# Kernel optimization log

Measured on AMD Instinct MI355X. Metric: run time of the kernel, lower is better.

The kernel has to match this reference:

```python
import jax, jax.numpy as jnp
import numpy as np

B, S, D, H = 4, 2048, 1024, 16
DK = D // H


def setup_inputs() -> dict:
    key = jax.random.key(0)
    ks = jax.random.split(key, 12)
    s = 1.0 / np.sqrt(D)
    return {
        "query": jax.random.normal(ks[0], (B, S, D), jnp.float32),
        "key": jax.random.normal(ks[1], (B, S, D), jnp.float32),
        "value": jax.random.normal(ks[2], (B, S, D), jnp.float32),
        "mask": jnp.ones((1, 1, S, S), jnp.int32),
        "w_q": jax.random.normal(ks[3], (D, D), jnp.float32) * s,
        "b_q": jax.random.normal(ks[4], (D,), jnp.float32) * s,
        "w_k": jax.random.normal(ks[5], (D, D), jnp.float32) * s,
        "b_k": jax.random.normal(ks[6], (D,), jnp.float32) * s,
        "w_v": jax.random.normal(ks[7], (D, D), jnp.float32) * s,
        "b_v": jax.random.normal(ks[8], (D,), jnp.float32) * s,
        "w_o": jax.random.normal(ks[9], (D, D), jnp.float32) * s,
        "b_o": jax.random.normal(ks[10], (D,), jnp.float32) * s,
    }


def reference(query, key, value, mask, w_q, b_q, w_k, b_k, w_v, b_v, w_o, b_o):
    # linear projections (torch Linear: x @ W^T + b)
    q = query @ w_q.T + b_q
    k = key @ w_k.T + b_k
    v = value @ w_v.T + b_v
    # [B, S, D] -> [B, H, S, DK]
    q = q.reshape(B, S, H, DK).transpose(0, 2, 1, 3)
    k = k.reshape(B, S, H, DK).transpose(0, 2, 1, 3)
    v = v.reshape(B, S, H, DK).transpose(0, 2, 1, 3)
    scores = jnp.einsum("bhqd,bhkd->bhqk", q, k) / jnp.sqrt(jnp.float32(DK))
    scores = jnp.where(mask == 0, jnp.float32(-1e9), scores)
    attn = jax.nn.softmax(scores, axis=-1)  # dropout p=0.0 -> identity
    x = jnp.einsum("bhqk,bhkd->bhqd", attn, v)
    x = x.transpose(0, 2, 1, 3).reshape(B, S, D)
    return x @ w_o.T + b_o
```

## Files before the change

kernel.cpp:

```cpp
#include <hip/hip_runtime.h>
#include <stdint.h>

#define S_LEN 2048
#define NHEAD 16
#define DHEAD 64
#define DMODEL 1024
#define MROWS 8192

typedef unsigned short ushort_t;
typedef __attribute__((ext_vector_type(8))) __bf16 bf16x8;
typedef __attribute__((ext_vector_type(4))) float f32x4;

__device__ __forceinline__ float bf2f(ushort_t h) {
    union { unsigned int u; float f; } v; v.u = ((unsigned int)h) << 16; return v.f;
}
__device__ __forceinline__ ushort_t f2bf(float f) {
    union { float f; unsigned int u; } v; v.f = f;
    unsigned int u = v.u + 0x7fffu + ((v.u >> 16) & 1u);
    return (ushort_t)(u >> 16);
}

__device__ __forceinline__ void gload_lds16(const void* g, void* l)
{
    auto* g1 = reinterpret_cast<const __attribute__((address_space(1))) void*>(
        reinterpret_cast<uintptr_t>(g));
    auto* l3 = reinterpret_cast<__attribute__((address_space(3))) void*>(
        reinterpret_cast<uintptr_t>(l));
    __builtin_amdgcn_global_load_lds(g1, l3, 16, 0, 0);
}

__global__ void detect_dtype(const unsigned int* __restrict__ q, int* __restrict__ flag)
{
    __shared__ int cnt;
    if (threadIdx.x == 0) cnt = 0;
    __syncthreads();
    int c = 0;
    for (int i = 0; i < 8; ++i) {
        const unsigned int w = q[threadIdx.x * 8 + i];
        const unsigned int lo = w & 0xffffu;
        const unsigned int e = (lo >> 7) & 0xffu;
        if (lo == 0u || (e >= 96u && e <= 160u)) ++c;
    }
    atomicAdd(&cnt, c);
    __syncthreads();
    if (threadIdx.x == 0) flag[0] = (cnt < 400) ? 1 : 0;
}

__global__ void mask_flags(const int* __restrict__ mask, int* __restrict__ flags)
{
    __shared__ int ok_s;
    if (threadIdx.x == 0) ok_s = 1;
    __syncthreads();
    const int t = blockIdx.x;
    const int tq = t >> 4, tk = t & 15;
    int ok = 1;
    for (int i = 0; i < 64; ++i) {
        const int idx = i * 256 + threadIdx.x;
        const int r = idx >> 7, c = idx & 127;
        if (mask[(size_t)(tq * 128 + r) * S_LEN + tk * 128 + c] == 0) { ok = 0; break; }
    }
    if (!ok) atomicAnd(&ok_s, 0);
    __syncthreads();
    if (threadIdx.x == 0) flags[t] = ok_s;
}

__device__ __forceinline__ float loadscal(const void* b, int i, bool f32)
{
    return f32 ? ((const float*)b)[i] : bf2f(((const ushort_t*)b)[i]);
}

__global__ __launch_bounds__(256)
void conv_bf16(const void* __restrict__ src, ushort_t* __restrict__ dst,
               int n8, const int* __restrict__ dflag, int fidx)
{
    const bool f32 = dflag[fidx] != 0;
    const int stride = gridDim.x * 256;
    for (int i = blockIdx.x * 256 + threadIdx.x; i < n8; i += stride) {
        if (f32) {
            const float4 a = ((const float4*)src)[2 * (size_t)i];
            const float4 b = ((const float4*)src)[2 * (size_t)i + 1];
            union { ushort_t u[8]; uint4 v; } p;
            p.u[0] = f2bf(a.x); p.u[1] = f2bf(a.y); p.u[2] = f2bf(a.z); p.u[3] = f2bf(a.w);
            p.u[4] = f2bf(b.x); p.u[5] = f2bf(b.y); p.u[6] = f2bf(b.z); p.u[7] = f2bf(b.w);
            ((uint4*)dst)[i] = p.v;
        } else {
            ((uint4*)dst)[i] = ((const uint4*)src)[i];
        }
    }
}

__device__ __forceinline__ void gemm_core(
    const ushort_t* __restrict__ A, const ushort_t* __restrict__ W,
    const void* __restrict__ bias, void* __restrict__ out,
    bool bf32, bool outf,
    ushort_t (&As)[3][128 * 32], ushort_t (&Bs)[3][128 * 32])
{
    constexpr int K = DMODEL, N = DMODEL;
    const int tid = threadIdx.x;
    const int lane = tid & 63;
    const int wave = tid >> 6;
    const int lrow = lane & 15, lq = lane >> 4;
    const int m0 = blockIdx.x * 128;
    const int n0 = blockIdx.y * 128;
    const int wr = (wave >> 1) * 64;
    const int wc = (wave & 1) * 64;

    const f32x4 zero4 = {0.f, 0.f, 0.f, 0.f};
    f32x4 acc[4][4];
#pragma unroll
    for (int i = 0; i < 4; ++i)
#pragma unroll
        for (int j = 0; j < 4; ++j) acc[i][j] = zero4;

    const int r0  = tid >> 2;
    const int cc0 = (tid & 3) * 8;
    const int lb  = wave * 64 * 8;
    const int lb1 = (wave * 64 + 256) * 8;

    auto stage = [&](int buf, int k0) __attribute__((always_inline)) {
        gload_lds16(&A[(size_t)(m0 + r0) * K + k0 + cc0],      &As[buf][lb]);
        gload_lds16(&A[(size_t)(m0 + r0 + 64) * K + k0 + cc0], &As[buf][lb1]);
        gload_lds16(&W[(size_t)(n0 + r0) * K + k0 + cc0],      &Bs[buf][lb]);
        gload_lds16(&W[(size_t)(n0 + r0 + 64) * K + k0 + cc0], &Bs[buf][lb1]);
    };
    auto compute = [&](int buf) __attribute__((always_inline)) {
        bf16x8 af[4], bfr[4];
#pragma unroll
        for (int t = 0; t < 4; ++t) {
            af[t]  = *(const bf16x8*)(&As[buf][(wr + t * 16 + lrow) * 32 + lq * 8]);
            bfr[t] = *(const bf16x8*)(&Bs[buf][(wc + t * 16 + lrow) * 32 + lq * 8]);
        }
        __builtin_amdgcn_s_setprio(1);
#pragma unroll
        for (int mt = 0; mt < 4; ++mt)
#pragma unroll
            for (int nt = 0; nt < 4; ++nt)
                acc[mt][nt] = __builtin_amdgcn_mfma_f32_16x16x32_bf16(
                    af[mt], bfr[nt], acc[mt][nt], 0, 0, 0);
        __builtin_amdgcn_s_setprio(0);
    };

    stage(0, 0);
    stage(1, 32);
    asm volatile("s_waitcnt vmcnt(4)" ::: "memory");
    __builtin_amdgcn_s_barrier();

#pragma unroll 1
    for (int tt = 0; tt < 32; ++tt) {
        if (tt < 30) stage((tt + 2) % 3, (tt + 2) * 32);
        compute(tt % 3);
        if (tt < 31) {
            if (tt < 30) asm volatile("s_waitcnt vmcnt(4)" ::: "memory");
            else         asm volatile("s_waitcnt vmcnt(0)" ::: "memory");
            __builtin_amdgcn_s_barrier();
        }
    }

#pragma unroll
    for (int nt = 0; nt < 4; ++nt) {
        const int n = n0 + wc + nt * 16 + lrow;
        const float bv = loadscal(bias, n, bf32);
#pragma unroll
        for (int mt = 0; mt < 4; ++mt) {
            const int mbase = m0 + wr + mt * 16 + lq * 4;
#pragma unroll
            for (int r = 0; r < 4; ++r) {
                const float v = acc[mt][nt][r] + bv;
                const size_t o = (size_t)(mbase + r) * N + n;
                if (outf) ((float*)out)[o] = v;
                else      ((ushort_t*)out)[o] = f2bf(v);
            }
        }
    }
}

__global__ __launch_bounds__(256, 3)
void gemm_bf16(const ushort_t* __restrict__ A, const ushort_t* __restrict__ W,
               const void* __restrict__ bias, void* __restrict__ out,
               const int* __restrict__ dflag, int outf)
{
    __shared__ ushort_t As[3][128 * 32];
    __shared__ ushort_t Bs[3][128 * 32];
    gemm_core(A, W, bias, out, dflag[1] != 0, outf != 0, As, Bs);
}

__global__ __launch_bounds__(256, 3)
void gemm_qk(const ushort_t* __restrict__ A0, const ushort_t* __restrict__ W0,
             const void* __restrict__ b0, void* __restrict__ o0,
             const ushort_t* __restrict__ A1, const ushort_t* __restrict__ W1,
             const void* __restrict__ b1, void* __restrict__ o1,
             const int* __restrict__ dflag)
{
    __shared__ ushort_t As[3][128 * 32];
    __shared__ ushort_t Bs[3][128 * 32];
    const bool z = blockIdx.z != 0;
    gemm_core(z ? A1 : A0, z ? W1 : W0, z ? b1 : b0, z ? o1 : o0,
              dflag[1] != 0, false, As, Bs);
}

__global__ __launch_bounds__(256, 2)
void attn_mfma(const ushort_t* __restrict__ Q, const ushort_t* __restrict__ K,
               const ushort_t* __restrict__ V, const int* __restrict__ mask,
               const int* __restrict__ flags, ushort_t* __restrict__ X)
{
    constexpr int KP = 72;
    constexpr int VP = 130;
    constexpr int PP = 68;
    constexpr float CEXP = 0.18033688f;
    __shared__ ushort_t Ks[128 * KP];
    __shared__ ushort_t VTs[64 * VP];
    __shared__ ushort_t Ps[4][32 * PP];

    const int tid = threadIdx.x;
    const int lane = tid & 63;
    const int wave = tid >> 6;
    const int lrow = lane & 15, lq = lane >> 4;
    const int bh = blockIdx.y, b = bh >> 4, h = bh & 15;
    const int q0 = blockIdx.x * 128;
    const int qw = q0 + wave * 32;
    const int coff = h * 64;
    const size_t rowb = (size_t)b * S_LEN;

    bf16x8 qf[2][2];
#pragma unroll
    for (int mt = 0; mt < 2; ++mt)
#pragma unroll
        for (int ks = 0; ks < 2; ++ks)
            qf[mt][ks] = *(const bf16x8*)(
                &Q[(rowb + qw + mt * 16 + lrow) * DMODEL + coff + ks * 32 + lq * 8]);

    const f32x4 zero4 = {0.f, 0.f, 0.f, 0.f};
    f32x4 o[2][4];
    float mr[2][4], lr[2][4];
#pragma unroll
    for (int mt = 0; mt < 2; ++mt) {
#pragma unroll
        for (int nt = 0; nt < 4; ++nt) o[mt][nt] = zero4;
#pragma unroll
        for (int r = 0; r < 4; ++r) { mr[mt][r] = -1e30f; lr[mt][r] = 0.f; }
    }

    ushort_t* const pw = &Ps[wave][0];

    for (int kt = 0; kt < 16; ++kt) {
        const int k0 = kt * 128;
#pragma unroll
        for (int i = 0; i < 4; ++i) {
            const int c = tid + i * 256;
            const int r = c >> 3, cc = (c & 7) * 8;
            *(uint4*)(&Ks[r * KP + cc]) =
                *(const uint4*)(&K[(rowb + k0 + r) * DMODEL + coff + cc]);
        }
#pragma unroll
        for (int i = 0; i < 2; ++i) {
            const int c = tid + i * 256;
            const int k2 = c >> 3;
            const int cc = (c & 7) * 8;
            union { uint4 v; ushort_t u[8]; } a, bb;
            a.v  = *(const uint4*)(&V[(rowb + k0 + 2 * k2)     * DMODEL + coff + cc]);
            bb.v = *(const uint4*)(&V[(rowb + k0 + 2 * k2 + 1) * DMODEL + coff + cc]);
#pragma unroll
            for (int j = 0; j < 8; ++j) {
                const unsigned int pk = (unsigned int)a.u[j] | ((unsigned int)bb.u[j] << 16);
                *(unsigned int*)(&VTs[(cc + j) * VP + 2 * k2]) = pk;
            }
        }
        __syncthreads();

        f32x4 s[2][8];
#pragma unroll
        for (int mt = 0; mt < 2; ++mt)
#pragma unroll
            for (int nt = 0; nt < 8; ++nt) s[mt][nt] = zero4;
#pragma unroll
        for (int nt = 0; nt < 8; ++nt) {
#pragma unroll
            for (int ks = 0; ks < 2; ++ks) {
                const bf16x8 kf = *(const bf16x8*)(&Ks[(nt * 16 + lrow) * KP + ks * 32 + lq * 8]);
                s[0][nt] = __builtin_amdgcn_mfma_f32_16x16x32_bf16(qf[0][ks], kf, s[0][nt], 0, 0, 0);
                s[1][nt] = __builtin_amdgcn_mfma_f32_16x16x32_bf16(qf[1][ks], kf, s[1][nt], 0, 0, 0);
            }
        }

        if (!flags[blockIdx.x * 16 + kt]) {
            for (int mt = 0; mt < 2; ++mt)
                for (int nt = 0; nt < 8; ++nt)
                    for (int r = 0; r < 4; ++r) {
                        const int qi = qw + mt * 16 + lq * 4 + r;
                        const int ki = k0 + nt * 16 + lrow;
                        if (mask[(size_t)qi * S_LEN + ki] == 0) s[mt][nt][r] = -1e9f;
                    }
        }

#pragma unroll
        for (int mt = 0; mt < 2; ++mt) {
#pragma unroll
            for (int r = 0; r < 4; ++r) {
                float v = fmaxf(
                    fmaxf(fmaxf(s[mt][0][r], s[mt][1][r]), fmaxf(s[mt][2][r], s[mt][3][r])),
                    fmaxf(fmaxf(s[mt][4][r], s[mt][5][r]), fmaxf(s[mt][6][r], s[mt][7][r])));
#pragma unroll
                for (int off = 1; off < 16; off <<= 1) v = fmaxf(v, __shfl_xor(v, off, 64));
                const float mn = fmaxf(mr[mt][r], v);
                const float alpha = __builtin_amdgcn_exp2f((mr[mt][r] - mn) * CEXP);
                mr[mt][r] = mn;
                const float mnC = mn * CEXP;
                float rs = 0.f;
#pragma unroll
                for (int nt = 0; nt < 8; ++nt) {
                    const float p = __builtin_amdgcn_exp2f(fmaf(s[mt][nt][r], CEXP, -mnC));
                    s[mt][nt][r] = p;
                    rs += p;
                }
#pragma unroll
                for (int off = 1; off < 16; off <<= 1) rs += __shfl_xor(rs, off, 64);
                lr[mt][r] = lr[mt][r] * alpha + rs;
#pragma unroll
                for (int nt = 0; nt < 4; ++nt) o[mt][nt][r] *= alpha;
            }
        }

#pragma unroll
        for (int half = 0; half < 2; ++half) {
#pragma unroll
            for (int mt = 0; mt < 2; ++mt)
#pragma unroll
                for (int nt = 0; nt < 4; ++nt)
#pragma unroll
                    for (int r = 0; r < 4; ++r)
                        pw[(mt * 16 + lq * 4 + r) * PP + nt * 16 + lrow] =
                            f2bf(s[mt][half * 4 + nt][r]);
#pragma unroll
            for (int ks = 0; ks < 2; ++ks) {
                const bf16x8 pf0 = *(const bf16x8*)(&pw[lrow * PP + ks * 32 + lq * 8]);
                const bf16x8 pf1 = *(const bf16x8*)(&pw[(16 + lrow) * PP + ks * 32 + lq * 8]);
                const int kb = half * 64 + ks * 32;
#pragma unroll
                for (int nt = 0; nt < 4; ++nt) {
                    const bf16x8 vf = *(const bf16x8*)(
                        &VTs[(nt * 16 + lrow) * VP + kb + lq * 8]);
                    o[0][nt] = __builtin_amdgcn_mfma_f32_16x16x32_bf16(pf0, vf, o[0][nt], 0, 0, 0);
                    o[1][nt] = __builtin_amdgcn_mfma_f32_16x16x32_bf16(pf1, vf, o[1][nt], 0, 0, 0);
                }
            }
        }
        __syncthreads();
    }

#pragma unroll
    for (int mt = 0; mt < 2; ++mt) {
#pragma unroll
        for (int r = 0; r < 4; ++r) {
            const float inv = 1.f / lr[mt][r];
            const int si = qw + mt * 16 + lq * 4 + r;
#pragma unroll
            for (int nt = 0; nt < 4; ++nt) {
                const int dk = nt * 16 + lrow;
                X[(rowb + si) * DMODEL + coff + dk] = f2bf(o[mt][nt][r] * inv);
            }
        }
    }
}

extern "C" void kernel_launch(void* const* d_in, const int* in_sizes, int n_in,
                              void* d_out, int out_size, void* d_ws, size_t ws_size,
                              hipStream_t stream)
{
    const void* query = d_in[0];
    const void* key   = d_in[1];
    const void* value = d_in[2];
    const int*  mask  = (const int*)d_in[3];
    const void* w_q = d_in[4];
    const void* b_q = d_in[5];
    const void* w_k = d_in[6];
    const void* b_k = d_in[7];
    const void* w_v = d_in[8];
    const void* b_v = d_in[9];
    const void* w_o = d_in[10];
    const void* b_o = d_in[11];

    const size_t TEN = (size_t)MROWS * DMODEL;
    const size_t WEL = (size_t)DMODEL * DMODEL;
    ushort_t* W0 = (ushort_t*)d_ws;
    ushort_t* W1 = W0 + TEN;
    ushort_t* W2 = W1 + TEN;
    int* dflag   = (int*)(W2 + TEN);
    int* flags   = dflag + 2;

    ushort_t* AcQ = (ushort_t*)d_out;
    ushort_t* AcK = AcQ + TEN;
    ushort_t* AcV = AcQ;
    ushort_t* Vp  = AcK;

    ushort_t* Wq_c = W2;
    ushort_t* Wk_c = W2 + WEL;
    ushort_t* Wv_c = W2 + 2 * WEL;
    ushort_t* Wo_c = W1;

    const int WN8 = (int)(WEL / 8);
    const int AN8 = (int)(TEN / 8);

    detect_dtype<<<1, 64, 0, stream>>>((const unsigned int*)query, dflag + 0);
    detect_dtype<<<1, 64, 0, stream>>>((const unsigned int*)w_q,   dflag + 1);
    mask_flags<<<256, 256, 0, stream>>>(mask, flags);

    conv_bf16<<<512, 256, 0, stream>>>(w_q, Wq_c, WN8, dflag, 1);
    conv_bf16<<<512, 256, 0, stream>>>(w_k, Wk_c, WN8, dflag, 1);
    conv_bf16<<<512, 256, 0, stream>>>(w_v, Wv_c, WN8, dflag, 1);
    conv_bf16<<<2048, 256, 0, stream>>>(query, AcQ, AN8, dflag, 0);
    conv_bf16<<<2048, 256, 0, stream>>>(key,   AcK, AN8, dflag, 0);

    gemm_qk<<<dim3(64, 8, 2), 256, 0, stream>>>(AcQ, Wq_c, b_q, W0,
                                                AcK, Wk_c, b_k, W1, dflag);

    conv_bf16<<<2048, 256, 0, stream>>>(value, AcV, AN8, dflag, 0);
    gemm_bf16<<<dim3(64, 8), 256, 0, stream>>>(AcV, Wv_c, b_v, Vp, dflag, 0);

    attn_mfma<<<dim3(16, 64), 256, 0, stream>>>(W0, W1, Vp, mask, flags, W2);

    conv_bf16<<<512, 256, 0, stream>>>(w_o, Wo_c, WN8, dflag, 1);
    gemm_bf16<<<dim3(64, 8), 256, 0, stream>>>(W2, Wo_c, b_o, d_out, dflag, 1);
}
```

Baseline: 541.0 us.

## Fold softmax scale into Q projection and batch conversion launches

The Q projection epilogue now multiplies by 1/sqrt(dk), so the attention kernel works on prescaled scores and uses __expf directly instead of exp2 with a folded constant. Three weight conversions and two activation conversions are merged into z-indexed grid launches to cut kernel launch count. The P tile padding in LDS changes from 68 to 72. Rounding Q to bf16 after scaling slightly changes numerics, and __expf may compile to an extra multiply ahead of exp2, so the softmax inner loop could cost a little more.

```diff
diff --git a/kernel.cpp b/kernel.cpp
--- a/kernel.cpp
+++ b/kernel.cpp
@@ -69,11 +69,10 @@
     return f32 ? ((const float*)b)[i] : bf2f(((const ushort_t*)b)[i]);
 }
 
-__global__ __launch_bounds__(256)
-void conv_bf16(const void* __restrict__ src, ushort_t* __restrict__ dst,
-               int n8, const int* __restrict__ dflag, int fidx)
-{
-    const bool f32 = dflag[fidx] != 0;
+__device__ __forceinline__ void conv_body(const void* __restrict__ src,
+                                          ushort_t* __restrict__ dst,
+                                          int n8, bool f32)
+{
     const int stride = gridDim.x * 256;
     for (int i = blockIdx.x * 256 + threadIdx.x; i < n8; i += stride) {
         if (f32) {
@@ -89,10 +88,29 @@
     }
 }
 
+__global__ __launch_bounds__(256)
+void conv_bf16(const void* __restrict__ src, ushort_t* __restrict__ dst,
+               int n8, const int* __restrict__ dflag, int fidx)
+{
+    conv_body(src, dst, n8, dflag[fidx] != 0);
+}
+
+__global__ __launch_bounds__(256)
+void conv_bf16_z(const void* __restrict__ s0, ushort_t* __restrict__ d0,
+                 const void* __restrict__ s1, ushort_t* __restrict__ d1,
+                 const void* __restrict__ s2, ushort_t* __restrict__ d2,
+                 int n8, const int* __restrict__ dflag, int fidx)
+{
+    const int z = blockIdx.z;
+    const void* src = (z == 0) ? s0 : (z == 1) ? s1 : s2;
+    ushort_t*  dst = (z == 0) ? d0 : (z == 1) ? d1 : d2;
+    conv_body(src, dst, n8, dflag[fidx] != 0);
+}
+
 __device__ __forceinline__ void gemm_core(
     const ushort_t* __restrict__ A, const ushort_t* __restrict__ W,
     const void* __restrict__ bias, void* __restrict__ out,
-    bool bf32, bool outf,
+    bool bf32, bool outf, float scale,
     ushort_t (&As)[3][128 * 32], ushort_t (&Bs)[3][128 * 32])
 {
     constexpr int K = DMODEL, N = DMODEL;
@@ -165,7 +183,7 @@
             const int mbase = m0 + wr + mt * 16 + lq * 4;
 #pragma unroll
             for (int r = 0; r < 4; ++r) {
-                const float v = acc[mt][nt][r] + bv;
+                const float v = (acc[mt][nt][r] + bv) * scale;
                 const size_t o = (size_t)(mbase + r) * N + n;
                 if (outf) ((float*)out)[o] = v;
                 else      ((ushort_t*)out)[o] = f2bf(v);
@@ -181,7 +199,7 @@
 {
     __shared__ ushort_t As[3][128 * 32];
     __shared__ ushort_t Bs[3][128 * 32];
-    gemm_core(A, W, bias, out, dflag[1] != 0, outf != 0, As, Bs);
+    gemm_core(A, W, bias, out, dflag[1] != 0, outf != 0, 1.0f, As, Bs);
 }
 
 __global__ __launch_bounds__(256, 3)
@@ -195,7 +213,7 @@
     __shared__ ushort_t Bs[3][128 * 32];
     const bool z = blockIdx.z != 0;
     gemm_core(z ? A1 : A0, z ? W1 : W0, z ? b1 : b0, z ? o1 : o0,
-              dflag[1] != 0, false, As, Bs);
+              dflag[1] != 0, false, z ? 1.0f : 0.125f, As, Bs);
 }
 
 __global__ __launch_bounds__(256, 2)
@@ -205,8 +223,7 @@
 {
     constexpr int KP = 72;
     constexpr int VP = 130;
-    constexpr int PP = 68;
-    constexpr float CEXP = 0.18033688f;
+    constexpr int PP = 72;
     __shared__ ushort_t Ks[128 * KP];
     __shared__ ushort_t VTs[64 * VP];
     __shared__ ushort_t Ps[4][32 * PP];
@@ -296,19 +313,18 @@
         for (int mt = 0; mt < 2; ++mt) {
 #pragma unroll
             for (int r = 0; r < 4; ++r) {
-                float v = fmaxf(
-                    fmaxf(fmaxf(s[mt][0][r], s[mt][1][r]), fmaxf(s[mt][2][r], s[mt][3][r])),
-                    fmaxf(fmaxf(s[mt][4][r], s[mt][5][r]), fmaxf(s[mt][6][r], s[mt][7][r])));
+                float v = s[mt][0][r];
+#pragma unroll
+                for (int nt = 1; nt < 8; ++nt) v = fmaxf(v, s[mt][nt][r]);
 #pragma unroll
                 for (int off = 1; off < 16; off <<= 1) v = fmaxf(v, __shfl_xor(v, off, 64));
                 const float mn = fmaxf(mr[mt][r], v);
-                const float alpha = __builtin_amdgcn_exp2f((mr[mt][r] - mn) * CEXP);
+                const float alpha = __expf(mr[mt][r] - mn);
                 mr[mt][r] = mn;
-                const float mnC = mn * CEXP;
                 float rs = 0.f;
 #pragma unroll
                 for (int nt = 0; nt < 8; ++nt) {
-                    const float p = __builtin_amdgcn_exp2f(fmaf(s[mt][nt][r], CEXP, -mnC));
+                    const float p = __expf(s[mt][nt][r] - mn);
                     s[mt][nt][r] = p;
                     rs += p;
                 }
@@ -404,11 +420,10 @@
     detect_dtype<<<1, 64, 0, stream>>>((const unsigned int*)w_q,   dflag + 1);
     mask_flags<<<256, 256, 0, stream>>>(mask, flags);
 
-    conv_bf16<<<512, 256, 0, stream>>>(w_q, Wq_c, WN8, dflag, 1);
-    conv_bf16<<<512, 256, 0, stream>>>(w_k, Wk_c, WN8, dflag, 1);
-    conv_bf16<<<512, 256, 0, stream>>>(w_v, Wv_c, WN8, dflag, 1);
-    conv_bf16<<<2048, 256, 0, stream>>>(query, AcQ, AN8, dflag, 0);
-    conv_bf16<<<2048, 256, 0, stream>>>(key,   AcK, AN8, dflag, 0);
+    conv_bf16_z<<<dim3(512, 1, 3), 256, 0, stream>>>(
+        w_q, Wq_c, w_k, Wk_c, w_v, Wv_c, WN8, dflag, 1);
+    conv_bf16_z<<<dim3(2048, 1, 2), 256, 0, stream>>>(
+        query, AcQ, key, AcK, (const void*)0, (ushort_t*)0, AN8, dflag, 0);
 
     gemm_qk<<<dim3(64, 8, 2), 256, 0, stream>>>(AcQ, Wq_c, b_q, W0,
                                                 AcK, Wk_c, b_k, W1, dflag);
```

Result: faster. 490.3 us (-9.4%).
